# Performance work log

Hardware: AMD Instinct MI355X
Metric: run time of the kernel (lower is better)

Reference implementation:

```python
import jax, jax.numpy as jnp
import numpy as np

C = 64        # number of classes (rows of mu)
K = 64        # int(d * overlap_ratio) = int(128 * 0.5)
ALPHA = 1.0   # margin


def _pairdist(mu, x):
    # Euclidean distance from every center to every sample: [C, N]
    d2 = (mu * mu).sum(-1)[:, None] + (x * x).sum(-1)[None, :] - 2.0 * (mu @ x.T)
    return jnp.sqrt(jnp.maximum(d2, 0.0))


def setup_inputs() -> dict:
    key = jax.random.key(0)
    k1, k2, k3 = jax.random.split(key, 3)
    N, D = 131072, 256
    x = jax.random.normal(k1, (N, D), dtype=jnp.float32)
    y = jax.random.randint(k2, (N, 3), 0, C)
    # ensure every class 0..C-1 is present with ~equal counts (matches torch.unique)
    y = y.at[:, 2].set(jnp.arange(N) % C)
    mu = jax.random.normal(k3, (C, D), dtype=jnp.float32)
    return {"x": x, "y": y, "mu": mu}


def reference(x, y, mu):
    labels = y[:, 2]                                     # [N]
    D = _pairdist(mu, x)                                 # [C, N]
    mask = labels[None, :] == jnp.arange(C)[:, None]     # [C, N] class membership

    # pos: per class c, K LARGEST distances from center c to its own samples
    pos_vals = jax.lax.top_k(jnp.where(mask, D, -jnp.inf), K)[0]  # [C, K]
    pos_mean = pos_vals.mean(-1)                                  # [C]

    # neg: for each sample-class c2, K SMALLEST distances from every center c1
    def neg_for_class(m):  # m: [N] bool mask for class c2
        vals = jax.lax.top_k(jnp.where(m[None, :], -D, -jnp.inf), K)[0]  # [C, K]
        return (-vals).mean(-1)  # [C] smallest-K mean per center c1

    negM = jax.lax.map(neg_for_class, mask)              # [C2, C1]

    hinge = jnp.maximum(ALPHA + pos_mean[None, :] - negM, 0.0)  # [C2, C1]
    offdiag = 1.0 - jnp.eye(C, dtype=hinge.dtype)
    loss = (hinge * offdiag).sum() / x.shape[0]
    return loss
```

## Files before the change

### kernel.cpp

```cpp
#include <hip/hip_runtime.h>
#include <math.h>


#define DDIM 256
#define CC 64
#define KSEL 64
#define TPTS 256
#define KC 32
#define XSTR 260
#define MSTR 68
#define SELN 2048

__global__ __launch_bounds__(128) void zeroK(int* cnts) {
  cnts[threadIdx.x] = 0;
}

__global__ __launch_bounds__(256) void countK(const int* __restrict__ y, int* cnt, int N) {
  int i = blockIdx.x * 256 + threadIdx.x;
  if (i < N) atomicAdd(&cnt[y[3 * i + 2] & (CC - 1)], 1);
}

__global__ void scanK(const int* __restrict__ cnt, int* base) {
  if (threadIdx.x == 0) {
    int s = 0;
    for (int i = 0; i < CC; ++i) { base[i] = s; s += cnt[i]; }
  }
}

__global__ __launch_bounds__(256) void fillK(const int* __restrict__ y, const int* __restrict__ base,
                                             int* cnt2, int* idxs, int N) {
  int i = blockIdx.x * 256 + threadIdx.x;
  if (i < N) {
    int m = y[3 * i + 2] & (CC - 1);
    int r = atomicAdd(&cnt2[m], 1);
    idxs[base[m] + r] = i;
  }
}

__global__ __launch_bounds__(256) void distK(const float* __restrict__ x, const float* __restrict__ mu,
                                             const int* __restrict__ idxs, float* __restrict__ Dg, int N) {
  __shared__ __align__(16) float xT[KC][XSTR];
  __shared__ __align__(16) float muT[KC][MSTR];
  __shared__ int pid[TPTS];
  __shared__ float xn2[TPTS];
  __shared__ float mun2[CC];
  const int t = threadIdx.x;
  const int wgp0 = blockIdx.x * TPTS;
  pid[t] = idxs[wgp0 + t];

  float acc[8][8];
  #pragma unroll
  for (int a = 0; a < 8; ++a)
    #pragma unroll
    for (int b = 0; b < 8; ++b) acc[a][b] = 0.f;
  float xn2r = 0.f, mun2r = 0.f;

  const int q = t & 7, pr = t >> 3;
  const int cs = t >> 2, qs = t & 3;
  const int p0 = (t & 31) * 4;
  const int c0 = (t >> 5) * 8;

  for (int ch = 0; ch < DDIM / KC; ++ch) {
    const int dbase = ch * KC;
    __syncthreads();
    #pragma unroll
    for (int r = 0; r < 8; ++r) {
      const int p = r * 32 + pr;
      const float4 v = *reinterpret_cast<const float4*>(x + (size_t)pid[p] * DDIM + dbase + 4 * q);
      xT[4 * q + 0][p] = v.x; xT[4 * q + 1][p] = v.y;
      xT[4 * q + 2][p] = v.z; xT[4 * q + 3][p] = v.w;
    }
    #pragma unroll
    for (int r = 0; r < 2; ++r) {
      const int q2 = qs + 4 * r;
      const float4 v = *reinterpret_cast<const float4*>(mu + cs * DDIM + dbase + 4 * q2);
      muT[4 * q2 + 0][cs] = v.x; muT[4 * q2 + 1][cs] = v.y;
      muT[4 * q2 + 2][cs] = v.z; muT[4 * q2 + 3][cs] = v.w;
    }
    __syncthreads();
    #pragma unroll 8
    for (int dd = 0; dd < KC; ++dd) { const float xv = xT[dd][t]; xn2r = fmaf(xv, xv, xn2r); }
    if (t < CC) {
      #pragma unroll 8
      for (int dd = 0; dd < KC; ++dd) { const float mv = muT[dd][t]; mun2r = fmaf(mv, mv, mun2r); }
    }
    #pragma unroll 4
    for (int dd = 0; dd < KC; ++dd) {
      const float4 xa = *reinterpret_cast<const float4*>(&xT[dd][p0]);
      const float4 xb = *reinterpret_cast<const float4*>(&xT[dd][p0 + 128]);
      const float4 ma = *reinterpret_cast<const float4*>(&muT[dd][c0]);
      const float4 mb = *reinterpret_cast<const float4*>(&muT[dd][c0 + 4]);
      const float xs[8] = {xa.x, xa.y, xa.z, xa.w, xb.x, xb.y, xb.z, xb.w};
      const float ms[8] = {ma.x, ma.y, ma.z, ma.w, mb.x, mb.y, mb.z, mb.w};
      #pragma unroll
      for (int ci = 0; ci < 8; ++ci)
        #pragma unroll
        for (int pj = 0; pj < 8; ++pj)
          acc[ci][pj] = fmaf(ms[ci], xs[pj], acc[ci][pj]);
    }
  }
  xn2[t] = xn2r;
  if (t < CC) mun2[t] = mun2r;
  __syncthreads();

  #pragma unroll
  for (int ci = 0; ci < 8; ++ci) {
    const int c = c0 + ci;
    const float mn = mun2[c];
    #pragma unroll
    for (int h = 0; h < 2; ++h) {
      const int pb = p0 + h * 128;
      float4 o;
      float* op = &o.x;
      #pragma unroll
      for (int j = 0; j < 4; ++j) {
        const float d2 = mn + xn2[pb + j] - 2.f * acc[ci][4 * h + j];
        op[j] = sqrtf(fmaxf(d2, 0.f));
      }
      *reinterpret_cast<float4*>(Dg + (size_t)c * N + wgp0 + pb) = o;
    }
  }
}

__global__ __launch_bounds__(128) void selK(const float* __restrict__ Dg, const int* __restrict__ cnt,
                                            const int* __restrict__ base, float* __restrict__ posM,
                                            float* __restrict__ neg, int N) {
  __shared__ __align__(16) unsigned int keys[SELN];
  __shared__ unsigned int sh_lo, sh_hi;
  __shared__ int sh_cnt[2];
  __shared__ float sh_sum[2];
  const int c = blockIdx.x, m = blockIdx.y;
  const int t = threadIdx.x;
  const int w = t >> 6, lane = t & 63;
  const bool diag = (c == m);
  int cm = cnt[m]; if (cm > SELN) cm = SELN;
  const int bm = base[m];
  const float* src = Dg + (size_t)c * N + bm;
  const int cm4 = (cm + 3) & ~3;

  unsigned int kmin = 0xFFFFFFFFu, kmax = 0u;
  for (int i = t; i < cm4; i += 128) {
    unsigned int key = 0xFFFFFFFFu;
    if (i < cm) {
      const unsigned int b = __float_as_uint(src[i]);
      key = diag ? ~b : b;
      kmin = min(kmin, key); kmax = max(kmax, key);
    }
    keys[i] = key;
  }
  #pragma unroll
  for (int off = 32; off > 0; off >>= 1) {
    kmin = min(kmin, (unsigned int)__shfl_xor((int)kmin, off, 64));
    kmax = max(kmax, (unsigned int)__shfl_xor((int)kmax, off, 64));
  }
  if (lane == 0) { sh_cnt[w] = (int)kmin; sh_sum[w] = __uint_as_float(kmax); }
  __syncthreads();
  if (t == 0) {
    sh_lo = min((unsigned int)sh_cnt[0], (unsigned int)sh_cnt[1]);
    sh_hi = max(__float_as_uint(sh_sum[0]), __float_as_uint(sh_sum[1]));
  }

  for (;;) {
    __syncthreads();
    const unsigned int lo = sh_lo, hi = sh_hi;
    if (lo >= hi) break;
    const unsigned int mid = lo + ((hi - lo) >> 1);
    int cl = 0;
    for (int i4 = t * 4; i4 < cm4; i4 += 512) {
      const uint4 kv = *reinterpret_cast<const uint4*>(&keys[i4]);
      cl += (int)(kv.x <= mid) + (int)(kv.y <= mid) + (int)(kv.z <= mid) + (int)(kv.w <= mid);
    }
    #pragma unroll
    for (int off = 32; off > 0; off >>= 1) cl += __shfl_xor(cl, off, 64);
    if (lane == 0) sh_cnt[w] = cl;
    __syncthreads();
    if (t == 0) {
      if (sh_cnt[0] + sh_cnt[1] >= KSEL) sh_hi = mid; else sh_lo = mid + 1;
    }
  }
  const unsigned int kth = sh_lo;

  int cl = 0; float sl = 0.f;
  for (int i4 = t * 4; i4 < cm4; i4 += 512) {
    const uint4 kv = *reinterpret_cast<const uint4*>(&keys[i4]);
    const unsigned int ks[4] = {kv.x, kv.y, kv.z, kv.w};
    #pragma unroll
    for (int j = 0; j < 4; ++j) {
      if (ks[j] < kth) { ++cl; sl += __uint_as_float(diag ? ~ks[j] : ks[j]); }
    }
  }
  #pragma unroll
  for (int off = 32; off > 0; off >>= 1) {
    cl += __shfl_xor(cl, off, 64);
    sl += __shfl_xor(sl, off, 64);
  }
  if (lane == 0) { sh_cnt[w] = cl; sh_sum[w] = sl; }
  __syncthreads();
  if (t == 0) {
    const int totc = sh_cnt[0] + sh_cnt[1];
    const float tots = sh_sum[0] + sh_sum[1];
    const float kval = __uint_as_float(diag ? ~kth : kth);
    const float mval = (tots + (float)(KSEL - totc) * kval) * (1.0f / KSEL);
    if (diag) posM[c] = mval; else neg[m * CC + c] = mval;
  }
}

__global__ __launch_bounds__(256) void lossK(const float* __restrict__ posM, const float* __restrict__ neg,
                                             float* __restrict__ out, int N) {
  __shared__ float red[256];
  const int t = threadIdx.x;
  float s = 0.f;
  for (int idx = t; idx < CC * CC; idx += 256) {
    const int m = idx >> 6, c = idx & 63;
    if (m != c) {
      const float h = 1.0f + posM[c] - neg[idx];
      s += fmaxf(h, 0.0f);
    }
  }
  red[t] = s;
  __syncthreads();
  for (int off = 128; off > 0; off >>= 1) {
    if (t < off) red[t] += red[t + off];
    __syncthreads();
  }
  if (t == 0) out[0] = red[0] / (float)N;
}

__global__ void wsFailK(float* out) {
  if (threadIdx.x == 0) out[0] = -1.0e30f;
}

extern "C" void kernel_launch(void* const* d_in, const int* in_sizes, int n_in,
                              void* d_out, int out_size, void* d_ws, size_t ws_size,
                              hipStream_t stream) {
  const float* x  = (const float*)d_in[0];
  const int*   y  = (const int*)d_in[1];
  const float* mu = (const float*)d_in[2];
  float* out = (float*)d_out;
  const int N = in_sizes[0] / DDIM;

  const size_t need = (size_t)557056 + (size_t)CC * (size_t)N * 4;
  if (ws_size < need) {
    hipLaunchKernelGGL(wsFailK, dim3(1), dim3(64), 0, stream, out);
    return;
  }
  char* w = (char*)d_ws;
  int*   cnt  = (int*)(w);
  int*   cnt2 = (int*)(w + 256);
  int*   base = (int*)(w + 512);
  float* posM = (float*)(w + 768);
  float* neg  = (float*)(w + 1024);
  int*   idxs = (int*)(w + 32768);
  float* Dg   = (float*)(w + 557056);

  hipLaunchKernelGGL(zeroK, dim3(1), dim3(128), 0, stream, cnt);
  hipLaunchKernelGGL(countK, dim3((N + 255) / 256), dim3(256), 0, stream, y, cnt, N);
  hipLaunchKernelGGL(scanK, dim3(1), dim3(64), 0, stream, cnt, base);
  hipLaunchKernelGGL(fillK, dim3((N + 255) / 256), dim3(256), 0, stream, y, base, cnt2, idxs, N);
  hipLaunchKernelGGL(distK, dim3(N / TPTS), dim3(256), 0, stream, x, mu, idxs, Dg, N);
  hipLaunchKernelGGL(selK, dim3(CC, CC), dim3(128), 0, stream, Dg, cnt, base, posM, neg, N);
  hipLaunchKernelGGL(lossK, dim3(1), dim3(256), 0, stream, posM, neg, out, N);
}
```

Baseline: 343.7 us.

## Compute center-sample dot products with split-bf16 MFMA instead of scalar FMA

The distance kernel's FP32 FMA outer product is replaced by MFMA 16x16x32 bf16 instructions. Each float is split into high and low bf16 parts, and three MFMAs (hh, hl, lh) approximate FP32 precision. The shared-memory layout changes to row-major bf16 tiles, and the squared norms are reduced with lane shuffles. The goal is to move the GEMM-like work onto the matrix cores, at the cost of conversion overhead, scattered scalar output stores, and a small loss of precision that could affect top-k ordering.

```diff
diff --git a/kernel.cpp b/kernel.cpp
--- a/kernel.cpp
+++ b/kernel.cpp
@@ -6,10 +6,21 @@
 #define CC 64
 #define KSEL 64
 #define TPTS 256
-#define KC 32
-#define XSTR 260
-#define MSTR 68
+#define XS 48
 #define SELN 2048
+
+typedef short s4v __attribute__((ext_vector_type(4)));
+typedef short s8v __attribute__((ext_vector_type(8)));
+typedef float f4v __attribute__((ext_vector_type(4)));
+
+__device__ __forceinline__ void cvt_split(float f, short& h, short& l) {
+  const unsigned int u = __float_as_uint(f);
+  const unsigned int hb = (u + 0x7FFFu + ((u >> 16) & 1u)) >> 16;
+  h = (short)hb;
+  const float rem = f - __uint_as_float(hb << 16);
+  const unsigned int ur = __float_as_uint(rem);
+  l = (short)((ur + 0x7FFFu + ((ur >> 16) & 1u)) >> 16);
+}
 
 __global__ __launch_bounds__(128) void zeroK(int* cnts) {
   cnts[threadIdx.x] = 0;
@@ -39,85 +50,123 @@
 
 __global__ __launch_bounds__(256) void distK(const float* __restrict__ x, const float* __restrict__ mu,
                                              const int* __restrict__ idxs, float* __restrict__ Dg, int N) {
-  __shared__ __align__(16) float xT[KC][XSTR];
-  __shared__ __align__(16) float muT[KC][MSTR];
+  __shared__ __align__(16) short xh[TPTS][XS];
+  __shared__ __align__(16) short xl[TPTS][XS];
+  __shared__ __align__(16) short mh[CC][XS];
+  __shared__ __align__(16) short ml[CC][XS];
   __shared__ int pid[TPTS];
   __shared__ float xn2[TPTS];
-  __shared__ float mun2[CC];
+  __shared__ float mn2[CC];
+
   const int t = threadIdx.x;
   const int wgp0 = blockIdx.x * TPTS;
   pid[t] = idxs[wgp0 + t];
 
-  float acc[8][8];
-  #pragma unroll
-  for (int a = 0; a < 8; ++a)
-    #pragma unroll
-    for (int b = 0; b < 8; ++b) acc[a][b] = 0.f;
-  float xn2r = 0.f, mun2r = 0.f;
-
-  const int q = t & 7, pr = t >> 3;
-  const int cs = t >> 2, qs = t & 3;
-  const int p0 = (t & 31) * 4;
-  const int c0 = (t >> 5) * 8;
-
-  for (int ch = 0; ch < DDIM / KC; ++ch) {
-    const int dbase = ch * KC;
+  const int q = t & 7,  pr = t >> 3;
+  const int q2 = t & 3, mm = t >> 2;
+  const int w = t >> 6, l = t & 63;
+  const int lr = l & 15, lk = l >> 4;
+
+  f4v acc[4][4];
+  #pragma unroll
+  for (int a = 0; a < 4; ++a)
+    #pragma unroll
+    for (int b = 0; b < 4; ++b) acc[a][b] = (f4v)0.f;
+  float xnacc[8] = {0.f, 0.f, 0.f, 0.f, 0.f, 0.f, 0.f, 0.f};
+  float mnacc = 0.f;
+
+  __syncthreads();
+  int pidr[8];
+  #pragma unroll
+  for (int r = 0; r < 8; ++r) pidr[r] = pid[r * 32 + pr];
+
+  for (int ch = 0; ch < 8; ++ch) {
+    const int kb = ch * 32;
+    if (ch) __syncthreads();
+    #pragma unroll
+    for (int r = 0; r < 8; ++r) {
+      const float4 v = *reinterpret_cast<const float4*>(x + (size_t)pidr[r] * DDIM + kb + q * 4);
+      const float vs[4] = {v.x, v.y, v.z, v.w};
+      s4v hv, lv;
+      float s2 = 0.f;
+      #pragma unroll
+      for (int j = 0; j < 4; ++j) {
+        short hj, lj; cvt_split(vs[j], hj, lj);
+        hv[j] = hj; lv[j] = lj;
+        s2 = fmaf(vs[j], vs[j], s2);
+      }
+      xnacc[r] += s2;
+      const int p = r * 32 + pr;
+      *reinterpret_cast<s4v*>(&xh[p][q * 4]) = hv;
+      *reinterpret_cast<s4v*>(&xl[p][q * 4]) = lv;
+    }
+    {
+      const float* msrc = mu + (size_t)mm * DDIM + kb + q2 * 8;
+      const float4 va = *reinterpret_cast<const float4*>(msrc);
+      const float4 vb = *reinterpret_cast<const float4*>(msrc + 4);
+      const float vs[8] = {va.x, va.y, va.z, va.w, vb.x, vb.y, vb.z, vb.w};
+      s4v h0, h1, l0, l1;
+      #pragma unroll
+      for (int j = 0; j < 4; ++j) {
+        short hj, lj; cvt_split(vs[j], hj, lj);
+        h0[j] = hj; l0[j] = lj;
+        mnacc = fmaf(vs[j], vs[j], mnacc);
+      }
+      #pragma unroll
+      for (int j = 0; j < 4; ++j) {
+        short hj, lj; cvt_split(vs[4 + j], hj, lj);
+        h1[j] = hj; l1[j] = lj;
+        mnacc = fmaf(vs[4 + j], vs[4 + j], mnacc);
+      }
+      *reinterpret_cast<s4v*>(&mh[mm][q2 * 8])     = h0;
+      *reinterpret_cast<s4v*>(&mh[mm][q2 * 8 + 4]) = h1;
+      *reinterpret_cast<s4v*>(&ml[mm][q2 * 8])     = l0;
+      *reinterpret_cast<s4v*>(&ml[mm][q2 * 8 + 4]) = l1;
+    }
     __syncthreads();
-    #pragma unroll
-    for (int r = 0; r < 8; ++r) {
-      const int p = r * 32 + pr;
-      const float4 v = *reinterpret_cast<const float4*>(x + (size_t)pid[p] * DDIM + dbase + 4 * q);
-      xT[4 * q + 0][p] = v.x; xT[4 * q + 1][p] = v.y;
-      xT[4 * q + 2][p] = v.z; xT[4 * q + 3][p] = v.w;
-    }
-    #pragma unroll
-    for (int r = 0; r < 2; ++r) {
-      const int q2 = qs + 4 * r;
-      const float4 v = *reinterpret_cast<const float4*>(mu + cs * DDIM + dbase + 4 * q2);
-      muT[4 * q2 + 0][cs] = v.x; muT[4 * q2 + 1][cs] = v.y;
-      muT[4 * q2 + 2][cs] = v.z; muT[4 * q2 + 3][cs] = v.w;
-    }
-    __syncthreads();
-    #pragma unroll 8
-    for (int dd = 0; dd < KC; ++dd) { const float xv = xT[dd][t]; xn2r = fmaf(xv, xv, xn2r); }
-    if (t < CC) {
-      #pragma unroll 8
-      for (int dd = 0; dd < KC; ++dd) { const float mv = muT[dd][t]; mun2r = fmaf(mv, mv, mun2r); }
-    }
-    #pragma unroll 4
-    for (int dd = 0; dd < KC; ++dd) {
-      const float4 xa = *reinterpret_cast<const float4*>(&xT[dd][p0]);
-      const float4 xb = *reinterpret_cast<const float4*>(&xT[dd][p0 + 128]);
-      const float4 ma = *reinterpret_cast<const float4*>(&muT[dd][c0]);
-      const float4 mb = *reinterpret_cast<const float4*>(&muT[dd][c0 + 4]);
-      const float xs[8] = {xa.x, xa.y, xa.z, xa.w, xb.x, xb.y, xb.z, xb.w};
-      const float ms[8] = {ma.x, ma.y, ma.z, ma.w, mb.x, mb.y, mb.z, mb.w};
-      #pragma unroll
-      for (int ci = 0; ci < 8; ++ci)
-        #pragma unroll
-        for (int pj = 0; pj < 8; ++pj)
-          acc[ci][pj] = fmaf(ms[ci], xs[pj], acc[ci][pj]);
-    }
-  }
-  xn2[t] = xn2r;
-  if (t < CC) mun2[t] = mun2r;
-  __syncthreads();
-
-  #pragma unroll
-  for (int ci = 0; ci < 8; ++ci) {
-    const int c = c0 + ci;
-    const float mn = mun2[c];
-    #pragma unroll
-    for (int h = 0; h < 2; ++h) {
-      const int pb = p0 + h * 128;
-      float4 o;
-      float* op = &o.x;
-      #pragma unroll
-      for (int j = 0; j < 4; ++j) {
-        const float d2 = mn + xn2[pb + j] - 2.f * acc[ci][4 * h + j];
-        op[j] = sqrtf(fmaxf(d2, 0.f));
-      }
-      *reinterpret_cast<float4*>(Dg + (size_t)c * N + wgp0 + pb) = o;
+    s8v ah[4], al_[4];
+    #pragma unroll
+    for (int mt = 0; mt < 4; ++mt) {
+      ah[mt]  = *reinterpret_cast<const s8v*>(&mh[mt * 16 + lr][lk * 8]);
+      al_[mt] = *reinterpret_cast<const s8v*>(&ml[mt * 16 + lr][lk * 8]);
+    }
+    #pragma unroll
+    for (int nt = 0; nt < 4; ++nt) {
+      const int prow = w * 64 + nt * 16 + lr;
+      const s8v bh = *reinterpret_cast<const s8v*>(&xh[prow][lk * 8]);
+      const s8v bl = *reinterpret_cast<const s8v*>(&xl[prow][lk * 8]);
+      #pragma unroll
+      for (int mt = 0; mt < 4; ++mt) {
+        acc[mt][nt] = __builtin_amdgcn_mfma_f32_16x16x32_bf16(ah[mt],  bh, acc[mt][nt], 0, 0, 0);
+        acc[mt][nt] = __builtin_amdgcn_mfma_f32_16x16x32_bf16(ah[mt],  bl, acc[mt][nt], 0, 0, 0);
+        acc[mt][nt] = __builtin_amdgcn_mfma_f32_16x16x32_bf16(al_[mt], bh, acc[mt][nt], 0, 0, 0);
+      }
+    }
+  }
+  #pragma unroll
+  for (int r = 0; r < 8; ++r) {
+    float s = xnacc[r];
+    s += __shfl_xor(s, 1, 64); s += __shfl_xor(s, 2, 64); s += __shfl_xor(s, 4, 64);
+    if (q == 0) xn2[r * 32 + pr] = s;
+  }
+  {
+    float s = mnacc;
+    s += __shfl_xor(s, 1, 64); s += __shfl_xor(s, 2, 64);
+    if (q2 == 0) mn2[mm] = s;
+  }
+  __syncthreads();
+  #pragma unroll
+  for (int mt = 0; mt < 4; ++mt) {
+    #pragma unroll
+    for (int r = 0; r < 4; ++r) {
+      const int m = mt * 16 + lk * 4 + r;
+      const float mn = mn2[m];
+      #pragma unroll
+      for (int nt = 0; nt < 4; ++nt) {
+        const int p = w * 64 + nt * 16 + lr;
+        const float d2 = mn + xn2[p] - 2.f * acc[mt][nt][r];
+        Dg[(size_t)m * N + wgp0 + p] = sqrtf(fmaxf(d2, 0.f));
+      }
     }
   }
 }
```

New measurement: 331.6 us. 3.5% less time.
